# Optimization experiments

Measured on AMD Instinct MI355X. Metric: run time of the kernel, lower is better.

Reference implementation:

```python
import jax, jax.numpy as jnp
import numpy as np

HEADS = 8
DIM_HEAD = 64
INNER = HEADS * DIM_HEAD  # 512
EPS = 1e-6


def layer_norm(x, gamma, beta):
    mu = jnp.mean(x, axis=-1, keepdims=True)
    var = jnp.var(x, axis=-1, keepdims=True)
    return (x - mu) * jax.lax.rsqrt(var + EPS) * gamma + beta


def setup_inputs() -> dict:
    key = jax.random.key(0)
    ks = jax.random.split(key, 8)
    b, n = 2, 2048
    s = lambda d: 1.0 / np.sqrt(d)
    return {
        "x": jax.random.normal(ks[0], (b, n, INNER), dtype=jnp.float32),
        # weights stored input-major: y = x @ W
        "w_qkv": jax.random.normal(ks[1], (INNER, 3 * INNER), dtype=jnp.float32) * s(INNER),
        "w_out": jax.random.normal(ks[2], (INNER, INNER), dtype=jnp.float32) * s(INNER),
        "b_out": jax.random.normal(ks[3], (INNER,), dtype=jnp.float32) * 0.01,
        "w_ff1": jax.random.normal(ks[4], (INNER, 4 * INNER), dtype=jnp.float32) * s(INNER),
        "w_ff2": jax.random.normal(ks[5], (4 * INNER, INNER), dtype=jnp.float32) * s(4 * INNER),
        "g1": jnp.ones((INNER,), dtype=jnp.float32),
        "be1": jnp.zeros((INNER,), dtype=jnp.float32),
        "g2": jnp.ones((INNER,), dtype=jnp.float32),
        "be2": jnp.zeros((INNER,), dtype=jnp.float32),
    }


def reference(x, w_qkv, w_out, b_out, w_ff1, w_ff2, g1, be1, g2, be2):
    b, n, _ = x.shape
    scale = DIM_HEAD ** (-0.5)
    qkv = x @ w_qkv  # [b, n, 3*inner]
    qkv = qkv.reshape(b, n, 3, HEADS, DIM_HEAD)
    q = qkv[:, :, 0].transpose(0, 2, 1, 3)  # [b, h, n, d]
    k = qkv[:, :, 1].transpose(0, 2, 1, 3)
    v = qkv[:, :, 2].transpose(0, 2, 1, 3)
    dots = jnp.einsum('bhqd,bhkd->bhqk', q, k) * scale
    attn = jax.nn.softmax(dots, axis=-1)
    out = jnp.einsum('bhqk,bhkd->bhqd', attn, v)
    out = out.transpose(0, 2, 1, 3).reshape(b, n, INNER)
    out = out @ w_out + b_out
    attn_res = layer_norm(x + out, g1, be1)
    # NOTE: no activation between the two FFN linears (faithful to source)
    ff = (attn_res @ w_ff1) @ w_ff2
    return layer_norm(attn_res + ff, g2, be2)
```

## Files before the change

kernel.cpp:

```cpp
#include <hip/hip_runtime.h>
#include <hip/hip_bf16.h>
#include <cstdint>
#include <cstddef>
#include <math.h>

#define HEADS 8
#define DHEAD 64
#define INNER 512
#define BATCH 2
#define SEQ   2048
#define MROWS (BATCH*SEQ)
#define LN_EPS 1e-6f
#define KSPLIT 8
#define KCHUNK (SEQ/KSPLIT)
#define QSCALE 0.18033688011110918f

typedef unsigned short u16;
typedef __attribute__((ext_vector_type(8))) short short8;
typedef __attribute__((ext_vector_type(4))) short short4v;
typedef __attribute__((ext_vector_type(4))) float f32x4;

#define MFMA16(a,b,c) __builtin_amdgcn_mfma_f32_16x16x32_bf16((a),(b),(c),0,0,0)
#if __has_builtin(__builtin_amdgcn_mfma_f32_16x16x16bf16_1k)
#define HAVE_MFMA16K16 1
#define MFMA16K16(a,b,c) __builtin_amdgcn_mfma_f32_16x16x16bf16_1k((a),(b),(c),0,0,0)
#endif

__device__ __forceinline__ float bf2f(u16 u) {
    union { float f; uint32_t i; } x; x.i = ((uint32_t)u) << 16; return x.f;
}
__device__ __forceinline__ u16 f2bf(float f) {
    __hip_bfloat16 h = __float2bfloat16(f);
    return *reinterpret_cast<u16*>(&h);
}
__device__ __forceinline__ void gl_lds16(const void* g, void* l) {
    __builtin_amdgcn_global_load_lds(
        (const __attribute__((address_space(1))) void*)g,
        (__attribute__((address_space(3))) void*)l, 16, 0, 0);
}

__global__ void prep_kernel(const float* __restrict__ x, u16* __restrict__ x_b,
                            const float* __restrict__ w_qkv, u16* __restrict__ w_qkvT,
                            const float* __restrict__ w_out, u16* __restrict__ w_outT,
                            const float* __restrict__ w_ff1, u16* __restrict__ w_ff1T,
                            const float* __restrict__ w_ff2, u16* __restrict__ w_ff2T) {
    __shared__ float T[32][33];
    const int blk = blockIdx.x, tid = threadIdx.x;
    if (blk < 2048) {
        int i = blk * 256 + tid;
        float4 v = reinterpret_cast<const float4*>(x)[i];
        ushort4 o;
        o.x = f2bf(v.x); o.y = f2bf(v.y); o.z = f2bf(v.z); o.w = f2bf(v.w);
        reinterpret_cast<ushort4*>(x_b)[i] = o;
        return;
    }
    const float* B; u16* Bt; int K, N, t;
    if (blk < 2816)      { B = w_qkv; Bt = w_qkvT; K = 512;  N = 1536; t = blk - 2048; }
    else if (blk < 3072) { B = w_out; Bt = w_outT; K = 512;  N = 512;  t = blk - 2816; }
    else if (blk < 4096) { B = w_ff1; Bt = w_ff1T; K = 512;  N = 2048; t = blk - 3072; }
    else                 { B = w_ff2; Bt = w_ff2T; K = 2048; N = 512;  t = blk - 4096; }
    const int nb = N / 32;
    const int n0 = (t % nb) * 32, k0 = (t / nb) * 32;
    const int r = tid >> 3, c = (tid & 7) * 4;
    float4 v = *reinterpret_cast<const float4*>(&B[(size_t)(k0 + r) * N + n0 + c]);
    T[c + 0][r] = v.x; T[c + 1][r] = v.y; T[c + 2][r] = v.z; T[c + 3][r] = v.w;
    __syncthreads();
    ushort4 o;
    o.x = f2bf(T[r][c + 0]); o.y = f2bf(T[r][c + 1]);
    o.z = f2bf(T[r][c + 2]); o.w = f2bf(T[r][c + 3]);
    *reinterpret_cast<ushort4*>(&Bt[(size_t)(n0 + r) * K + k0 + c]) = o;
}

template<int BN, int BK, int EPI>
__global__ __launch_bounds__(256) void gemm_bt(const u16* __restrict__ A,
                                               const u16* __restrict__ Bt,
                                               u16* __restrict__ Cb,
                                               u16* __restrict__ Vt,
                                               int M, int N, int K) {
    constexpr int WN = BN / 2;
    constexpr int NT = WN / 16;
    constexpr int ACH = 128 * BK / 8;
    constexpr int BCH = BN * BK / 8;
    constexpr int CW = BK / 8;
    __shared__ u16 As[128 * BK];
    __shared__ u16 Bs[BN * BK];
    const int tid = threadIdx.x;
    const int wave = tid >> 6, lane = tid & 63;
    const int l15 = lane & 15, quad = lane >> 4;
    const int wm = (wave >> 1) * 64, wn = (wave & 1) * WN;
    const int row0 = blockIdx.y * 128, col0 = blockIdx.x * BN;

    int kbase = 0, kend = K;
    if (EPI == 3) {
        int chunk = K / gridDim.z;
        kbase = blockIdx.z * chunk; kend = kbase + chunk;
    }

    f32x4 acc[4][NT];
    #pragma unroll
    for (int mi = 0; mi < 4; ++mi)
        #pragma unroll
        for (int ni = 0; ni < NT; ++ni)
            #pragma unroll
            for (int e = 0; e < 4; ++e) acc[mi][ni][e] = 0.f;

    for (int k0 = kbase; k0 < kend; k0 += BK) {
        #pragma unroll
        for (int idx0 = 0; idx0 < ACH + BCH; idx0 += 256) {
            int idx = idx0 + tid;
            if (idx < ACH) {
                int r = idx / CW, ic = (idx % CW) * 8;
                gl_lds16(A + (size_t)(row0 + r) * K + k0 + ic, &As[idx * 8]);
            } else {
                int ib = idx - ACH;
                int r = ib / CW, ic = (ib % CW) * 8;
                gl_lds16(Bt + (size_t)(col0 + r) * K + k0 + ic, &Bs[ib * 8]);
            }
        }
        __syncthreads();

        #pragma unroll
        for (int ks2 = 0; ks2 < BK / 32; ++ks2) {
            short8 af[4], bfr[NT];
            #pragma unroll
            for (int mi = 0; mi < 4; ++mi)
                af[mi] = *reinterpret_cast<const short8*>(
                    &As[(wm + mi * 16 + l15) * BK + ks2 * 32 + quad * 8]);
            #pragma unroll
            for (int ni = 0; ni < NT; ++ni)
                bfr[ni] = *reinterpret_cast<const short8*>(
                    &Bs[(wn + ni * 16 + l15) * BK + ks2 * 32 + quad * 8]);
            #pragma unroll
            for (int mi = 0; mi < 4; ++mi)
                #pragma unroll
                for (int ni = 0; ni < NT; ++ni)
                    acc[mi][ni] = MFMA16(af[mi], bfr[ni], acc[mi][ni]);
        }
        __syncthreads();
    }

    #pragma unroll
    for (int mi = 0; mi < 4; ++mi)
        #pragma unroll
        for (int ni = 0; ni < NT; ++ni) {
            const int cc = col0 + wn + ni * 16 + l15;
            const int rr0 = row0 + wm + mi * 16 + quad * 4;
            if (EPI == 0) {
                #pragma unroll
                for (int r = 0; r < 4; ++r)
                    Cb[(size_t)(rr0 + r) * N + cc] = f2bf(acc[mi][ni][r]);
            } else if (EPI == 3) {
                u16* Cz = Cb + (size_t)blockIdx.z * M * N;
                #pragma unroll
                for (int r = 0; r < 4; ++r)
                    Cz[(size_t)(rr0 + r) * N + cc] = f2bf(acc[mi][ni][r]);
            } else {
                if (cc < 1024) {
                    const bool isq = (cc < 512);
                    size_t base = isq ? (size_t)cc
                                      : ((size_t)MROWS * 512 + cc - 512);
                    const float sc = isq ? QSCALE : 1.f;
                    #pragma unroll
                    for (int r = 0; r < 4; ++r)
                        Cb[base + (size_t)(rr0 + r) * 512] = f2bf(acc[mi][ni][r] * sc);
                } else {
                    int hh = (cc - 1024) >> 6, dd = (cc - 1024) & 63;
                    int bb = rr0 >> 11, srow = rr0 & 2047;
                    ushort4 o;
                    o.x = f2bf(acc[mi][ni][0]); o.y = f2bf(acc[mi][ni][1]);
                    o.z = f2bf(acc[mi][ni][2]); o.w = f2bf(acc[mi][ni][3]);
                    *reinterpret_cast<ushort4*>(
                        &Vt[(((size_t)(bb * 8 + hh) * 64 + dd) << 11) + srow]) = o;
                }
            }
        }
}

__global__ __launch_bounds__(256) void attn_kernel(const u16* __restrict__ qk_b,
                                                   const u16* __restrict__ vT_b,
                                                   u16* __restrict__ OpartB,
                                                   float* __restrict__ lpart) {
#ifdef HAVE_MFMA16K16
    __shared__ u16 SM[2 * 64 * 72];
    u16 (*Ks)[72] = (u16(*)[72])SM;
    u16 (*VT)[72] = (u16(*)[72])(SM + 64 * 72);
#else
    __shared__ u16 SM[64 * 64 + 2 * 64 * 72];
    u16 (*Qs)[64] = (u16(*)[64])SM;
    u16 (*Ks)[72] = (u16(*)[72])(SM + 64 * 64);
    u16 (*VT)[72] = (u16(*)[72])(SM + 64 * 64 + 64 * 72);
#endif

    const int tid = threadIdx.x;
    const int wave = tid >> 6, lane = tid & 63;
    const int l15 = lane & 15, quad = lane >> 4;
    const int qt = blockIdx.x, bh = blockIdx.y, ks = blockIdx.z;
    const int b = bh >> 3, h = bh & 7;
    const int w16 = wave * 16;
    const int r0 = tid >> 3, r1 = r0 + 32;
    const int ch = (tid & 7) * 8;
    constexpr int NT = KCHUNK / 64;

    const u16* qb = qk_b + (size_t)(b * SEQ + qt * 64) * 512 + h * 64;
    const u16* kb = qk_b + (size_t)MROWS * 512
                  + (size_t)(b * SEQ + ks * KCHUNK) * 512 + h * 64;
    const u16* vb = vT_b + (size_t)bh * 64 * 2048 + ks * KCHUNK;

    uint4 kr0 = *reinterpret_cast<const uint4*>(&kb[(size_t)r0 * 512 + ch]);
    uint4 kr1 = *reinterpret_cast<const uint4*>(&kb[(size_t)r1 * 512 + ch]);
    uint4 vr0 = *reinterpret_cast<const uint4*>(&vb[(size_t)r0 * 2048 + ch]);
    uint4 vr1 = *reinterpret_cast<const uint4*>(&vb[(size_t)r1 * 2048 + ch]);

#ifdef HAVE_MFMA16K16
    short8 qf[2];
    qf[0] = *reinterpret_cast<const short8*>(&qb[(size_t)(w16 + l15) * 512 + quad * 8]);
    qf[1] = *reinterpret_cast<const short8*>(&qb[(size_t)(w16 + l15) * 512 + 32 + quad * 8]);

    const short ONEB = (short)0x3F80;
    const short4v ones = {ONEB, ONEB, ONEB, ONEB};

    f32x4 oacc[4], lacc;
    #pragma unroll
    for (int di = 0; di < 4; ++di)
        #pragma unroll
        for (int e = 0; e < 4; ++e) oacc[di][e] = 0.f;
    #pragma unroll
    for (int e = 0; e < 4; ++e) lacc[e] = 0.f;

    for (int kt = 0; kt < NT; ++kt) {
        *reinterpret_cast<uint4*>(&Ks[r0][ch]) = kr0;
        *reinterpret_cast<uint4*>(&Ks[r1][ch]) = kr1;
        *reinterpret_cast<uint4*>(&VT[r0][ch]) = vr0;
        *reinterpret_cast<uint4*>(&VT[r1][ch]) = vr1;
        __syncthreads();

        if (kt + 1 < NT) {
            const u16* kb2 = kb + (size_t)(kt + 1) * 64 * 512;
            const u16* vb2 = vb + (kt + 1) * 64;
            kr0 = *reinterpret_cast<const uint4*>(&kb2[(size_t)r0 * 512 + ch]);
            kr1 = *reinterpret_cast<const uint4*>(&kb2[(size_t)r1 * 512 + ch]);
            vr0 = *reinterpret_cast<const uint4*>(&vb2[(size_t)r0 * 2048 + ch]);
            vr1 = *reinterpret_cast<const uint4*>(&vb2[(size_t)r1 * 2048 + ch]);
        }

        f32x4 sacc[4];
        #pragma unroll
        for (int ni = 0; ni < 4; ++ni)
            #pragma unroll
            for (int e = 0; e < 4; ++e) sacc[ni][e] = 0.f;
        {
            short8 kf[4], kf2[4];
            #pragma unroll
            for (int ni = 0; ni < 4; ++ni) {
                kf[ni]  = *reinterpret_cast<const short8*>(&Ks[ni * 16 + l15][quad * 8]);
                kf2[ni] = *reinterpret_cast<const short8*>(&Ks[ni * 16 + l15][32 + quad * 8]);
            }
            #pragma unroll
            for (int ni = 0; ni < 4; ++ni)
                sacc[ni] = MFMA16(kf[ni], qf[0], sacc[ni]);
            #pragma unroll
            for (int ni = 0; ni < 4; ++ni)
                sacc[ni] = MFMA16(kf2[ni], qf[1], sacc[ni]);
        }

        #pragma unroll
        for (int ni = 0; ni < 4; ++ni) {
            float p0 = exp2f(sacc[ni][0]);
            float p1 = exp2f(sacc[ni][1]);
            float p2 = exp2f(sacc[ni][2]);
            float p3 = exp2f(sacc[ni][3]);
            union { short4v v; uint32_t u[2]; } P;
            P.u[0] = __builtin_amdgcn_perm(__float_as_uint(p1),
                                           __float_as_uint(p0), 0x07060302u);
            P.u[1] = __builtin_amdgcn_perm(__float_as_uint(p3),
                                           __float_as_uint(p2), 0x07060302u);
            lacc = MFMA16K16(ones, P.v, lacc);
            #pragma unroll
            for (int di = 0; di < 4; ++di) {
                short4v vf = *reinterpret_cast<const short4v*>(
                    &VT[di * 16 + l15][ni * 16 + quad * 4]);
                oacc[di] = MFMA16K16(vf, P.v, oacc[di]);
            }
        }
        __syncthreads();
    }

    const size_t pbase = ((size_t)(ks * 16 + bh) * SEQ + qt * 64);
    if (lane < 16) lpart[pbase + w16 + lane] = lacc[0];

    float* OTf = (float*)SM;
    #pragma unroll
    for (int di = 0; di < 4; ++di)
        #pragma unroll
        for (int r = 0; r < 4; ++r)
            OTf[(di * 16 + quad * 4 + r) * 68 + w16 + l15] = oacc[di][r];
    __syncthreads();

    const int ql = tid >> 2, dseg = (tid & 3) * 16;
    u16 ov[16];
    #pragma unroll
    for (int i = 0; i < 16; ++i) ov[i] = f2bf(OTf[(dseg + i) * 68 + ql]);
    u16* op = &OpartB[(pbase + ql) * 64 + dseg];
    *reinterpret_cast<uint4*>(op)     = *reinterpret_cast<const uint4*>(ov);
    *reinterpret_cast<uint4*>(op + 8) = *reinterpret_cast<const uint4*>(ov + 8);
#else
    {
        #pragma unroll
        for (int j = 0; j < 2; ++j) {
            int idx = tid + j * 256;
            int r = idx >> 3, c = (idx & 7) * 8;
            *reinterpret_cast<uint4*>(&Qs[r][c]) =
                *reinterpret_cast<const uint4*>(&qb[(size_t)r * 512 + c]);
        }
    }
    __syncthreads();

    short8 qf[2];
    qf[0] = *reinterpret_cast<const short8*>(&Qs[w16 + l15][quad * 8]);
    qf[1] = *reinterpret_cast<const short8*>(&Qs[w16 + l15][32 + quad * 8]);

    f32x4 oacc[4];
    float lsum[4];
    #pragma unroll
    for (int di = 0; di < 4; ++di) {
        #pragma unroll
        for (int e = 0; e < 4; ++e) oacc[di][e] = 0.f;
        lsum[di] = 0.f;
    }

    for (int kt = 0; kt < NT; ++kt) {
        *reinterpret_cast<uint4*>(&Ks[r0][ch]) = kr0;
        *reinterpret_cast<uint4*>(&Ks[r1][ch]) = kr1;
        *reinterpret_cast<uint4*>(&VT[r0][ch]) = vr0;
        *reinterpret_cast<uint4*>(&VT[r1][ch]) = vr1;
        __syncthreads();

        if (kt + 1 < NT) {
            const u16* kb2 = kb + (size_t)(kt + 1) * 64 * 512;
            const u16* vb2 = vb + (kt + 1) * 64;
            kr0 = *reinterpret_cast<const uint4*>(&kb2[(size_t)r0 * 512 + ch]);
            kr1 = *reinterpret_cast<const uint4*>(&kb2[(size_t)r1 * 512 + ch]);
            vr0 = *reinterpret_cast<const uint4*>(&vb2[(size_t)r0 * 2048 + ch]);
            vr1 = *reinterpret_cast<const uint4*>(&vb2[(size_t)r1 * 2048 + ch]);
        }

        f32x4 sacc[4];
        #pragma unroll
        for (int ni = 0; ni < 4; ++ni)
            #pragma unroll
            for (int e = 0; e < 4; ++e) sacc[ni][e] = 0.f;
        #pragma unroll
        for (int ksk = 0; ksk < 2; ++ksk) {
            short8 kf[4];
            #pragma unroll
            for (int ni = 0; ni < 4; ++ni)
                kf[ni] = *reinterpret_cast<const short8*>(
                    &Ks[ni * 16 + l15][ksk * 32 + quad * 8]);
            #pragma unroll
            for (int ni = 0; ni < 4; ++ni)
                sacc[ni] = MFMA16(qf[ksk], kf[ni], sacc[ni]);
        }
        #pragma unroll
        for (int ni = 0; ni < 4; ++ni)
            #pragma unroll
            for (int r = 0; r < 4; ++r) {
                float p = exp2f(sacc[ni][r]);
                lsum[r] += p;
                Qs[w16 + quad * 4 + r][ni * 16 + l15] = f2bf(p);
            }
        #pragma unroll
        for (int ksk = 0; ksk < 2; ++ksk) {
            short8 pf = *reinterpret_cast<const short8*>(
                &Qs[w16 + l15][ksk * 32 + quad * 8]);
            #pragma unroll
            for (int di = 0; di < 4; ++di) {
                short8 vf = *reinterpret_cast<const short8*>(
                    &VT[di * 16 + l15][ksk * 32 + quad * 8]);
                oacc[di] = MFMA16(pf, vf, oacc[di]);
            }
        }
        __syncthreads();
    }

    const size_t pbase = ((size_t)(ks * 16 + bh) * SEQ + qt * 64);
    #pragma unroll
    for (int r = 0; r < 4; ++r) {
        float v = lsum[r];
        v += __shfl_xor(v, 1); v += __shfl_xor(v, 2);
        v += __shfl_xor(v, 4); v += __shfl_xor(v, 8);
        lsum[r] = v;
    }
    #pragma unroll
    for (int di = 0; di < 4; ++di)
        #pragma unroll
        for (int r = 0; r < 4; ++r)
            OpartB[(pbase + w16 + quad * 4 + r) * 64 + di * 16 + l15]
                = f2bf(oacc[di][r]);
    if (l15 == 0)
        #pragma unroll
        for (int r = 0; r < 4; ++r)
            lpart[pbase + w16 + quad * 4 + r] = lsum[r];
#endif
}

__global__ void attn_combine_kernel(const u16* __restrict__ OpartB,
                                    const float* __restrict__ lpart,
                                    u16* __restrict__ attn_b) {
    int i = blockIdx.x * 256 + threadIdx.x;
    int e = i * 4;
    int row = e >> 9;
    int c = e & 511;
    int h = c >> 6, d = c & 63;
    int b = row >> 11, srow = row & 2047;
    int bh = b * 8 + h;

    float ax = 0.f, ay = 0.f, az = 0.f, aw = 0.f, l = 0.f;
    #pragma unroll
    for (int ks = 0; ks < KSPLIT; ++ks) {
        size_t pk = (size_t)(ks * 16 + bh) * SEQ + srow;
        ushort4 o = *reinterpret_cast<const ushort4*>(&OpartB[pk * 64 + d]);
        ax += bf2f(o.x); ay += bf2f(o.y); az += bf2f(o.z); aw += bf2f(o.w);
        l += lpart[pk];
    }
    float li = 1.f / l;
    ushort4 o;
    o.x = f2bf(ax * li); o.y = f2bf(ay * li);
    o.z = f2bf(az * li); o.w = f2bf(aw * li);
    *reinterpret_cast<ushort4*>(&attn_b[(size_t)row * INNER + c]) = o;
}

template<bool A16, int NS>
__global__ __launch_bounds__(256) void ln_kernel(const void* __restrict__ a_,
                                                 const u16* __restrict__ s_,
                                                 size_t sstride,
                                                 const float* __restrict__ bias,
                                                 const float* __restrict__ g,
                                                 const float* __restrict__ be,
                                                 float* __restrict__ out32,
                                                 u16* __restrict__ out16) {
    const int tid = threadIdx.x, wave = tid >> 6, lane = tid & 63;
    const int row = blockIdx.x * 4 + wave;
    const size_t off = (size_t)row * INNER;

    float v[8];
    #pragma unroll
    for (int j = 0; j < 2; ++j) {
        const int c = j * 256 + lane * 4;
        if (A16) {
            ushort4 u = *reinterpret_cast<const ushort4*>((const u16*)a_ + off + c);
            v[j*4+0] = bf2f(u.x); v[j*4+1] = bf2f(u.y);
            v[j*4+2] = bf2f(u.z); v[j*4+3] = bf2f(u.w);
        } else {
            float4 u = *reinterpret_cast<const float4*>((const float*)a_ + off + c);
            v[j*4+0] = u.x; v[j*4+1] = u.y; v[j*4+2] = u.z; v[j*4+3] = u.w;
        }
        #pragma unroll
        for (int s = 0; s < NS; ++s) {
            ushort4 u = *reinterpret_cast<const ushort4*>(
                s_ + (size_t)s * sstride + off + c);
            v[j*4+0] += bf2f(u.x); v[j*4+1] += bf2f(u.y);
            v[j*4+2] += bf2f(u.z); v[j*4+3] += bf2f(u.w);
        }
        if (bias) {
            float4 u = *reinterpret_cast<const float4*>(bias + c);
            v[j*4+0] += u.x; v[j*4+1] += u.y; v[j*4+2] += u.z; v[j*4+3] += u.w;
        }
    }

    float s = 0.f;
    #pragma unroll
    for (int i = 0; i < 8; ++i) s += v[i];
    #pragma unroll
    for (int m = 1; m < 64; m <<= 1) s += __shfl_xor(s, m);
    const float mu = s * (1.f / INNER);

    float q = 0.f;
    #pragma unroll
    for (int i = 0; i < 8; ++i) { v[i] -= mu; q += v[i] * v[i]; }
    #pragma unroll
    for (int m = 1; m < 64; m <<= 1) q += __shfl_xor(q, m);
    const float rstd = rsqrtf(q * (1.f / INNER) + LN_EPS);

    #pragma unroll
    for (int j = 0; j < 2; ++j) {
        const int c = j * 256 + lane * 4;
        float4 gv = *reinterpret_cast<const float4*>(g + c);
        float4 bv = *reinterpret_cast<const float4*>(be + c);
        float y0 = v[j*4+0] * rstd * gv.x + bv.x;
        float y1 = v[j*4+1] * rstd * gv.y + bv.y;
        float y2 = v[j*4+2] * rstd * gv.z + bv.z;
        float y3 = v[j*4+3] * rstd * gv.w + bv.w;
        if (out32) {
            float4 o = {y0, y1, y2, y3};
            *reinterpret_cast<float4*>(out32 + off + c) = o;
        }
        if (out16) {
            ushort4 o;
            o.x = f2bf(y0); o.y = f2bf(y1); o.z = f2bf(y2); o.w = f2bf(y3);
            *reinterpret_cast<ushort4*>(out16 + off + c) = o;
        }
    }
}

extern "C" void kernel_launch(void* const* d_in, const int* in_sizes, int n_in,
                              void* d_out, int out_size, void* d_ws, size_t ws_size,
                              hipStream_t stream) {
    const float* x     = (const float*)d_in[0];
    const float* w_qkv = (const float*)d_in[1];
    const float* w_out = (const float*)d_in[2];
    const float* b_out = (const float*)d_in[3];
    const float* w_ff1 = (const float*)d_in[4];
    const float* w_ff2 = (const float*)d_in[5];
    const float* g1    = (const float*)d_in[6];
    const float* be1   = (const float*)d_in[7];
    const float* g2    = (const float*)d_in[8];
    const float* be2   = (const float*)d_in[9];
    float* out = (float*)d_out;

    char* W = (char*)d_ws;
    u16*   w_outT     = (u16*)  (W + 0);
    u16*   w_ff1T     = (u16*)  (W + 524288);
    u16*   w_ff2T     = (u16*)  (W + 2621440);
    u16*   qk_b       = (u16*)  (W + 4718592);
    u16*   projp      = (u16*)  (W + 4718592);
    u16*   vT_b       = (u16*)  (W + 13107200);
    u16*   attn_b     = (u16*)  (W + 13107200);
    u16*   attn_res_b = (u16*)  (W + 13107200);
    u16*   x_b        = (u16*)  (W + 17301504);
    u16*   w_qkvT     = (u16*)  (W + 21495808);
    float* lpart      = (float*)(W + 21495808);
    u16*   OpartB     = (u16*)  (W + 23068672);
    u16*   ff1_b      = (u16*)  (W + 17301504);
    u16*   ff2p       = (u16*)  (W + 34078720);

    prep_kernel<<<5120, 256, 0, stream>>>(x, x_b, w_qkv, w_qkvT, w_out, w_outT,
                                          w_ff1, w_ff1T, w_ff2, w_ff2T);

    gemm_bt<64, 64, 2><<<dim3(1536 / 64, MROWS / 128), 256, 0, stream>>>(
        x_b, w_qkvT, qk_b, vT_b, MROWS, 1536, INNER);

    attn_kernel<<<dim3(SEQ / 64, BATCH * HEADS, KSPLIT), 256, 0, stream>>>(
        qk_b, vT_b, OpartB, lpart);

    attn_combine_kernel<<<(MROWS * INNER / 4) / 256, 256, 0, stream>>>(
        OpartB, lpart, attn_b);

    gemm_bt<64, 64, 3><<<dim3(INNER / 64, MROWS / 128, 2), 256, 0, stream>>>(
        attn_b, w_outT, projp, nullptr, MROWS, INNER, INNER);

    ln_kernel<true, 2><<<MROWS / 4, 256, 0, stream>>>(
        x_b, projp, (size_t)MROWS * INNER, b_out, g1, be1, nullptr, attn_res_b);

    gemm_bt<128, 64, 0><<<dim3(2048 / 128, MROWS / 128), 256, 0, stream>>>(
        attn_res_b, w_ff1T, ff1_b, nullptr, MROWS, 2048, INNER);

    gemm_bt<64, 64, 3><<<dim3(INNER / 64, MROWS / 128, 4), 256, 0, stream>>>(
        ff1_b, w_ff2T, ff2p, nullptr, MROWS, INNER, 2048);

    ln_kernel<true, 4><<<MROWS / 4, 256, 0, stream>>>(
        attn_res_b, ff2p, (size_t)MROWS * INNER, nullptr, g2, be2, out, nullptr);
}
```

Measured before the change: 209.6 us.

## Drop attention KV split and fuse x bf16 conversion into QKV GEMM

Removes the split-K attention (KSPLIT=8) and its combine kernel. Each block now walks the full sequence and writes normalized output straight into attn_b. Separately, the x-to-bf16 conversion is folded into the QKV GEMM's A-tile load, and the first LayerNorm now reads x in fp32. This cuts two kernel launches and the partial-output traffic. In exchange, the attention grid is 8x smaller (512 blocks), which may underfill the GPU, and the A loads become synchronous register loads instead of direct-to-LDS loads.

```diff
diff --git a/kernel.cpp b/kernel.cpp
--- a/kernel.cpp
+++ b/kernel.cpp
@@ -11,8 +11,6 @@
 #define SEQ   2048
 #define MROWS (BATCH*SEQ)
 #define LN_EPS 1e-6f
-#define KSPLIT 8
-#define KCHUNK (SEQ/KSPLIT)
 #define QSCALE 0.18033688011110918f
 
 typedef unsigned short u16;
@@ -39,26 +37,17 @@
         (__attribute__((address_space(3))) void*)l, 16, 0, 0);
 }
 
-__global__ void prep_kernel(const float* __restrict__ x, u16* __restrict__ x_b,
-                            const float* __restrict__ w_qkv, u16* __restrict__ w_qkvT,
+__global__ void prep_kernel(const float* __restrict__ w_qkv, u16* __restrict__ w_qkvT,
                             const float* __restrict__ w_out, u16* __restrict__ w_outT,
                             const float* __restrict__ w_ff1, u16* __restrict__ w_ff1T,
                             const float* __restrict__ w_ff2, u16* __restrict__ w_ff2T) {
     __shared__ float T[32][33];
     const int blk = blockIdx.x, tid = threadIdx.x;
-    if (blk < 2048) {
-        int i = blk * 256 + tid;
-        float4 v = reinterpret_cast<const float4*>(x)[i];
-        ushort4 o;
-        o.x = f2bf(v.x); o.y = f2bf(v.y); o.z = f2bf(v.z); o.w = f2bf(v.w);
-        reinterpret_cast<ushort4*>(x_b)[i] = o;
-        return;
-    }
     const float* B; u16* Bt; int K, N, t;
-    if (blk < 2816)      { B = w_qkv; Bt = w_qkvT; K = 512;  N = 1536; t = blk - 2048; }
-    else if (blk < 3072) { B = w_out; Bt = w_outT; K = 512;  N = 512;  t = blk - 2816; }
-    else if (blk < 4096) { B = w_ff1; Bt = w_ff1T; K = 512;  N = 2048; t = blk - 3072; }
-    else                 { B = w_ff2; Bt = w_ff2T; K = 2048; N = 512;  t = blk - 4096; }
+    if (blk < 768)       { B = w_qkv; Bt = w_qkvT; K = 512;  N = 1536; t = blk; }
+    else if (blk < 1024) { B = w_out; Bt = w_outT; K = 512;  N = 512;  t = blk - 768; }
+    else if (blk < 2048) { B = w_ff1; Bt = w_ff1T; K = 512;  N = 2048; t = blk - 1024; }
+    else                 { B = w_ff2; Bt = w_ff2T; K = 2048; N = 512;  t = blk - 2048; }
     const int nb = N / 32;
     const int n0 = (t % nb) * 32, k0 = (t / nb) * 32;
     const int r = tid >> 3, c = (tid & 7) * 4;
@@ -71,8 +60,8 @@
     *reinterpret_cast<ushort4*>(&Bt[(size_t)(n0 + r) * K + k0 + c]) = o;
 }
 
-template<int BN, int BK, int EPI>
-__global__ __launch_bounds__(256) void gemm_bt(const u16* __restrict__ A,
+template<int BN, int BK, int EPI, bool AF32>
+__global__ __launch_bounds__(256) void gemm_bt(const void* __restrict__ A,
                                                const u16* __restrict__ Bt,
                                                u16* __restrict__ Cb,
                                                u16* __restrict__ Vt,
@@ -110,7 +99,18 @@
             int idx = idx0 + tid;
             if (idx < ACH) {
                 int r = idx / CW, ic = (idx % CW) * 8;
-                gl_lds16(A + (size_t)(row0 + r) * K + k0 + ic, &As[idx * 8]);
+                if (AF32) {
+                    const float* p = (const float*)A + (size_t)(row0 + r) * K + k0 + ic;
+                    float4 a = *reinterpret_cast<const float4*>(p);
+                    float4 b2 = *reinterpret_cast<const float4*>(p + 4);
+                    u16 t8[8] = {f2bf(a.x), f2bf(a.y), f2bf(a.z), f2bf(a.w),
+                                 f2bf(b2.x), f2bf(b2.y), f2bf(b2.z), f2bf(b2.w)};
+                    *reinterpret_cast<uint4*>(&As[idx * 8]) =
+                        *reinterpret_cast<const uint4*>(t8);
+                } else {
+                    gl_lds16((const u16*)A + (size_t)(row0 + r) * K + k0 + ic,
+                             &As[idx * 8]);
+                }
             } else {
                 int ib = idx - ACH;
                 int r = ib / CW, ic = (ib % CW) * 8;
@@ -178,8 +178,7 @@
 
 __global__ __launch_bounds__(256) void attn_kernel(const u16* __restrict__ qk_b,
                                                    const u16* __restrict__ vT_b,
-                                                   u16* __restrict__ OpartB,
-                                                   float* __restrict__ lpart) {
+                                                   u16* __restrict__ attn_b) {
 #ifdef HAVE_MFMA16K16
     __shared__ u16 SM[2 * 64 * 72];
     u16 (*Ks)[72] = (u16(*)[72])SM;
@@ -194,17 +193,16 @@
     const int tid = threadIdx.x;
     const int wave = tid >> 6, lane = tid & 63;
     const int l15 = lane & 15, quad = lane >> 4;
-    const int qt = blockIdx.x, bh = blockIdx.y, ks = blockIdx.z;
+    const int qt = blockIdx.x, bh = blockIdx.y;
     const int b = bh >> 3, h = bh & 7;
     const int w16 = wave * 16;
     const int r0 = tid >> 3, r1 = r0 + 32;
     const int ch = (tid & 7) * 8;
-    constexpr int NT = KCHUNK / 64;
+    constexpr int NT = SEQ / 64;
 
     const u16* qb = qk_b + (size_t)(b * SEQ + qt * 64) * 512 + h * 64;
-    const u16* kb = qk_b + (size_t)MROWS * 512
-                  + (size_t)(b * SEQ + ks * KCHUNK) * 512 + h * 64;
-    const u16* vb = vT_b + (size_t)bh * 64 * 2048 + ks * KCHUNK;
+    const u16* kb = qk_b + (size_t)MROWS * 512 + (size_t)b * SEQ * 512 + h * 64;
+    const u16* vb = vT_b + (size_t)bh * 64 * 2048;
 
     uint4 kr0 = *reinterpret_cast<const uint4*>(&kb[(size_t)r0 * 512 + ch]);
     uint4 kr1 = *reinterpret_cast<const uint4*>(&kb[(size_t)r1 * 512 + ch]);
@@ -285,8 +283,11 @@
         __syncthreads();
     }
 
-    const size_t pbase = ((size_t)(ks * 16 + bh) * SEQ + qt * 64);
-    if (lane < 16) lpart[pbase + w16 + lane] = lacc[0];
+    const float li = 1.f / lacc[0];
+    #pragma unroll
+    for (int di = 0; di < 4; ++di)
+        #pragma unroll
+        for (int e = 0; e < 4; ++e) oacc[di][e] *= li;
 
     float* OTf = (float*)SM;
     #pragma unroll
@@ -300,7 +301,7 @@
     u16 ov[16];
     #pragma unroll
     for (int i = 0; i < 16; ++i) ov[i] = f2bf(OTf[(dseg + i) * 68 + ql]);
-    u16* op = &OpartB[(pbase + ql) * 64 + dseg];
+    u16* op = &attn_b[(size_t)(b * SEQ + qt * 64 + ql) * INNER + h * 64 + dseg];
     *reinterpret_cast<uint4*>(op)     = *reinterpret_cast<const uint4*>(ov);
     *reinterpret_cast<uint4*>(op + 8) = *reinterpret_cast<const uint4*>(ov + 8);
 #else
@@ -382,51 +383,20 @@
         __syncthreads();
     }
 
-    const size_t pbase = ((size_t)(ks * 16 + bh) * SEQ + qt * 64);
     #pragma unroll
     for (int r = 0; r < 4; ++r) {
         float v = lsum[r];
         v += __shfl_xor(v, 1); v += __shfl_xor(v, 2);
         v += __shfl_xor(v, 4); v += __shfl_xor(v, 8);
-        lsum[r] = v;
+        lsum[r] = 1.f / v;
     }
     #pragma unroll
     for (int di = 0; di < 4; ++di)
         #pragma unroll
         for (int r = 0; r < 4; ++r)
-            OpartB[(pbase + w16 + quad * 4 + r) * 64 + di * 16 + l15]
-                = f2bf(oacc[di][r]);
-    if (l15 == 0)
-        #pragma unroll
-        for (int r = 0; r < 4; ++r)
-            lpart[pbase + w16 + quad * 4 + r] = lsum[r];
+            attn_b[(size_t)(b * SEQ + qt * 64 + w16 + quad * 4 + r) * INNER
+                   + h * 64 + di * 16 + l15] = f2bf(oacc[di][r] * lsum[r]);
 #endif
-}
-
-__global__ void attn_combine_kernel(const u16* __restrict__ OpartB,
-                                    const float* __restrict__ lpart,
-                                    u16* __restrict__ attn_b) {
-    int i = blockIdx.x * 256 + threadIdx.x;
-    int e = i * 4;
-    int row = e >> 9;
-    int c = e & 511;
-    int h = c >> 6, d = c & 63;
-    int b = row >> 11, srow = row & 2047;
-    int bh = b * 8 + h;
-
-    float ax = 0.f, ay = 0.f, az = 0.f, aw = 0.f, l = 0.f;
-    #pragma unroll
-    for (int ks = 0; ks < KSPLIT; ++ks) {
-        size_t pk = (size_t)(ks * 16 + bh) * SEQ + srow;
-        ushort4 o = *reinterpret_cast<const ushort4*>(&OpartB[pk * 64 + d]);
-        ax += bf2f(o.x); ay += bf2f(o.y); az += bf2f(o.z); aw += bf2f(o.w);
-        l += lpart[pk];
-    }
-    float li = 1.f / l;
-    ushort4 o;
-    o.x = f2bf(ax * li); o.y = f2bf(ay * li);
-    o.z = f2bf(az * li); o.w = f2bf(aw * li);
-    *reinterpret_cast<ushort4*>(&attn_b[(size_t)row * INNER + c]) = o;
 }
 
 template<bool A16, int NS>
@@ -524,37 +494,31 @@
     u16*   qk_b       = (u16*)  (W + 4718592);
     u16*   projp      = (u16*)  (W + 4718592);
     u16*   vT_b       = (u16*)  (W + 13107200);
-    u16*   attn_b     = (u16*)  (W + 13107200);
     u16*   attn_res_b = (u16*)  (W + 13107200);
-    u16*   x_b        = (u16*)  (W + 17301504);
+    u16*   attn_b     = (u16*)  (W + 17301504);
     u16*   w_qkvT     = (u16*)  (W + 21495808);
-    float* lpart      = (float*)(W + 21495808);
-    u16*   OpartB     = (u16*)  (W + 23068672);
-    u16*   ff1_b      = (u16*)  (W + 17301504);
-    u16*   ff2p       = (u16*)  (W + 34078720);
-
-    prep_kernel<<<5120, 256, 0, stream>>>(x, x_b, w_qkv, w_qkvT, w_out, w_outT,
+    u16*   ff1_b      = (u16*)  (W + 21495808);
+    u16*   ff2p       = (u16*)  (W + 38273024);
+
+    prep_kernel<<<3072, 256, 0, stream>>>(w_qkv, w_qkvT, w_out, w_outT,
                                           w_ff1, w_ff1T, w_ff2, w_ff2T);
 
-    gemm_bt<64, 64, 2><<<dim3(1536 / 64, MROWS / 128), 256, 0, stream>>>(
-        x_b, w_qkvT, qk_b, vT_b, MROWS, 1536, INNER);
-
-    attn_kernel<<<dim3(SEQ / 64, BATCH * HEADS, KSPLIT), 256, 0, stream>>>(
-        qk_b, vT_b, OpartB, lpart);
-
-    attn_combine_kernel<<<(MROWS * INNER / 4) / 256, 256, 0, stream>>>(
-        OpartB, lpart, attn_b);
-
-    gemm_bt<64, 64, 3><<<dim3(INNER / 64, MROWS / 128, 2), 256, 0, stream>>>(
+    gemm_bt<64, 64, 2, true><<<dim3(1536 / 64, MROWS / 128), 256, 0, stream>>>(
+        x, w_qkvT, qk_b, vT_b, MROWS, 1536, INNER);
+
+    attn_kernel<<<dim3(SEQ / 64, BATCH * HEADS), 256, 0, stream>>>(
+        qk_b, vT_b, attn_b);
+
+    gemm_bt<64, 64, 3, false><<<dim3(INNER / 64, MROWS / 128, 2), 256, 0, stream>>>(
         attn_b, w_outT, projp, nullptr, MROWS, INNER, INNER);
 
-    ln_kernel<true, 2><<<MROWS / 4, 256, 0, stream>>>(
-        x_b, projp, (size_t)MROWS * INNER, b_out, g1, be1, nullptr, attn_res_b);
-
-    gemm_bt<128, 64, 0><<<dim3(2048 / 128, MROWS / 128), 256, 0, stream>>>(
+    ln_kernel<false, 2><<<MROWS / 4, 256, 0, stream>>>(
+        x, projp, (size_t)MROWS * INNER, b_out, g1, be1, nullptr, attn_res_b);
+
+    gemm_bt<128, 64, 0, false><<<dim3(2048 / 128, MROWS / 128), 256, 0, stream>>>(
         attn_res_b, w_ff1T, ff1_b, nullptr, MROWS, 2048, INNER);
 
-    gemm_bt<64, 64, 3><<<dim3(INNER / 64, MROWS / 128, 4), 256, 0, stream>>>(
+    gemm_bt<64, 64, 3, false><<<dim3(INNER / 64, MROWS / 128, 4), 256, 0, stream>>>(
         ff1_b, w_ff2T, ff2p, nullptr, MROWS, INNER, 2048);
 
     ln_kernel<true, 4><<<MROWS / 4, 256, 0, stream>>>(
```

Result: slower. 214.4 us (+2.3%).
